# Kernel optimization log

Hardware: AMD Instinct MI355X
Metric: run time of the kernel (lower is better)

The kernel has to match this reference:

```python
import jax, jax.numpy as jnp
import numpy as np

N, F = 2048, 128
HEADS, OUT_DIM = 8, 8
ALPHA = 0.2  # tf.nn.leaky_relu default


def setup_inputs() -> dict:
    key = jax.random.key(0)
    k1, k2, k3, k4 = jax.random.split(key, 4)
    X = jax.random.normal(k1, (N, F), dtype=jnp.float32)
    A = jax.random.randint(k2, (N, N), 0, 2, dtype=jnp.int32)
    W = jax.random.normal(k3, (F, OUT_DIM * HEADS), dtype=jnp.float32) * (1.0 / np.sqrt(F))
    attn_kernel = jax.random.normal(k4, (2 * OUT_DIM, 1), dtype=jnp.float32) * 0.1
    return {"X": X, "A": A, "W": W, "attn_kernel": attn_kernel}


def reference(X, A, W, attn_kernel):
    # h: [N, heads, out_dim]
    h = (X @ W).reshape(N, HEADS, OUT_DIM)
    # tensordot(concat(h_i, h_j), a) == h_i @ a1 + h_j @ a2 (linear before leaky_relu),
    # so avoid materializing the [N,N,heads,2*out_dim] tile-concat tensor.
    a1 = attn_kernel[:OUT_DIM, 0]
    a2 = attn_kernel[OUT_DIM:, 0]
    s1 = jnp.einsum('nhd,d->nh', h, a1)  # [N, heads]
    s2 = jnp.einsum('nhd,d->nh', h, a2)  # [N, heads]
    e = jax.nn.leaky_relu(s1[:, None, :] + s2[None, :, :], ALPHA)  # [N, N, heads]
    mask = (A > 0).astype(e.dtype)[:, :, None]
    e = e * mask - 1e9 * (1.0 - mask)
    attention = jax.nn.softmax(e, axis=1)  # softmax over neighbor axis (axis=1), as in source
    # Faithful to source: einsum 'nij,njh->nih' contracts the HEAD axis
    # (attention [N,N,heads] with h [N,heads,out_dim]) -> [N, N, out_dim]
    h_prime = jnp.einsum('nij,njh->nih', attention, h)
    h_prime = h_prime.reshape(-1, OUT_DIM * HEADS)  # [N*N/heads, out_dim*heads]
    return jax.nn.leaky_relu(h_prime, ALPHA)
```

## Files before the change

### kernel.cpp

```cpp
#include <hip/hip_runtime.h>

#define NN      2048
#define FDIM    128
#define HEADS   8
#define ODIM    8
#define HID     64
#define ALPHA   0.2f

__device__ __forceinline__ float lrelu(float x) {
    return x > 0.f ? x : ALPHA * x;
}

__device__ __forceinline__ float rfl(float x) {
    return __int_as_float(__builtin_amdgcn_readfirstlane(__float_as_int(x)));
}

__global__ __launch_bounds__(64) void gat_prep(
        const float* __restrict__ X,
        const float* __restrict__ W,
        const float* __restrict__ ak,
        float* __restrict__ H,
        float* __restrict__ S1,
        float* __restrict__ S2) {
    const int n = blockIdx.x;
    const int t = threadIdx.x;

    __shared__ float Xs[FDIM];
    __shared__ float hs[HID];

    Xs[t]      = X[(size_t)n * FDIM + t];
    Xs[t + 64] = X[(size_t)n * FDIM + 64 + t];
    __syncthreads();

    float acc = 0.f;
    #pragma unroll 8
    for (int k = 0; k < FDIM; ++k)
        acc = fmaf(Xs[k], W[k * HID + t], acc);

    H[(size_t)n * HID + t] = acc;
    hs[t] = acc;
    __syncthreads();

    if (t < 16) {
        const int head = t & 7;
        const float* a = ak + ((t < 8) ? 0 : ODIM);
        float s = 0.f;
        #pragma unroll
        for (int d = 0; d < ODIM; ++d)
            s = fmaf(hs[head * ODIM + d], a[d], s);
        if (t < 8) S1[n * HEADS + head] = s;
        else       S2[n * HEADS + head] = s;
    }
}

__global__ __launch_bounds__(512, 4) void gat_fused(
        const int*   __restrict__ A,
        const float* __restrict__ H,
        const float* __restrict__ S1,
        const float* __restrict__ S2,
        float* __restrict__ out) {
    const int i    = blockIdx.x;
    const int t    = threadIdx.x;
    const int wave = t >> 6;
    const int lane = t & 63;

    __shared__ float hhS[HID];
    __shared__ float redL[8 * HEADS];
    __shared__ float LFs[HEADS];

    if (t < HID)
        hhS[t] = H[(size_t)i * HID + t];

    float s1r[HEADS];
    #pragma unroll
    for (int h = 0; h < HEADS; ++h)
        s1r[h] = rfl(S1[i * HEADS + h]);

    float p[4][HEADS];
    float ls[HEADS];
    #pragma unroll
    for (int h = 0; h < HEADS; ++h) ls[h] = 0.f;

    #pragma unroll
    for (int jj = 0; jj < 4; ++jj) {
        const int j = t + jj * 512;
        const int  msk_i = A[(size_t)i * NN + j];
        const float4 sa = *(const float4*)(S2 + j * HEADS);
        const float4 sb = *(const float4*)(S2 + j * HEADS + 4);
        const bool msk = msk_i > 0;
        const float s2v[8] = {sa.x, sa.y, sa.z, sa.w,
                              sb.x, sb.y, sb.z, sb.w};
        #pragma unroll
        for (int h = 0; h < HEADS; ++h) {
            const float x  = s1r[h] + s2v[h];
            const float pe = msk ? __expf(lrelu(x)) : 0.f;
            p[jj][h] = pe;
            ls[h]   += pe;
        }
    }

    #pragma unroll
    for (int h = 0; h < HEADS; ++h) {
        float v = ls[h];
        #pragma unroll
        for (int off = 32; off; off >>= 1)
            v += __shfl_xor(v, off);
        if (lane == 0) redL[wave * HEADS + h] = v;
    }
    __syncthreads();

    if (t < HEADS) {
        float v = 0.f;
        #pragma unroll
        for (int w = 0; w < 8; ++w)
            v += redL[w * HEADS + t];
        LFs[t] = v;
    }
    __syncthreads();

    float hh_s[HID];
    #pragma unroll
    for (int h = 0; h < HEADS; ++h) {
        const float inv = 1.0f / LFs[h];
        #pragma unroll
        for (int d = 0; d < ODIM; ++d)
            hh_s[h * ODIM + d] = rfl(hhS[h * ODIM + d] * inv);
    }

    #pragma unroll
    for (int jj = 0; jj < 4; ++jj) {
        const int j = t + jj * 512;

        float o[ODIM];
        #pragma unroll
        for (int d = 0; d < ODIM; ++d) o[d] = 0.f;
        #pragma unroll
        for (int h = 0; h < HEADS; ++h) {
            #pragma unroll
            for (int d = 0; d < ODIM; ++d)
                o[d] = fmaf(p[jj][h], hh_s[h * ODIM + d], o[d]);
        }

        const size_t base = ((size_t)i * NN + j) * ODIM;
        float4 o0, o1;
        o0.x = lrelu(o[0]); o0.y = lrelu(o[1]);
        o0.z = lrelu(o[2]); o0.w = lrelu(o[3]);
        o1.x = lrelu(o[4]); o1.y = lrelu(o[5]);
        o1.z = lrelu(o[6]); o1.w = lrelu(o[7]);
        *(float4*)(out + base)     = o0;
        *(float4*)(out + base + 4) = o1;
    }
}

extern "C" void kernel_launch(void* const* d_in, const int* in_sizes, int n_in,
                              void* d_out, int out_size, void* d_ws, size_t ws_size,
                              hipStream_t stream) {
    const float* X  = (const float*)d_in[0];
    const int*   A  = (const int*)  d_in[1];
    const float* W  = (const float*)d_in[2];
    const float* ak = (const float*)d_in[3];
    float* out = (float*)d_out;

    float* H  = (float*)d_ws;
    float* S1 = H  + (size_t)NN * HID;
    float* S2 = S1 + (size_t)NN * HEADS;

    gat_prep <<<NN,  64, 0, stream>>>(X, W, ak, H, S1, S2);
    gat_fused<<<NN, 512, 0, stream>>>(A, H, S1, S2, out);
}
```

Baseline: 185.4 us.

## Split fused attention kernel into row-sum and write kernels with finer blocks

Splits the single fused kernel into one kernel that computes the per-row softmax denominators and stores them in workspace, and another that recomputes the exponentials and writes output. The write kernel launches 8x more blocks, each thread producing one float4 of output instead of eight float4 for four columns. The aim is more parallelism and lower register pressure on the store-bound write phase. In exchange, the adjacency matrix and S2 are read twice, the exponentials are computed twice, and there is an extra kernel launch.

```diff
diff --git a/kernel.cpp b/kernel.cpp
--- a/kernel.cpp
+++ b/kernel.cpp
@@ -53,30 +53,23 @@
     }
 }
 
-__global__ __launch_bounds__(512, 4) void gat_fused(
+__global__ __launch_bounds__(512) void gat_rowsum(
         const int*   __restrict__ A,
-        const float* __restrict__ H,
         const float* __restrict__ S1,
         const float* __restrict__ S2,
-        float* __restrict__ out) {
+        float* __restrict__ LF) {
     const int i    = blockIdx.x;
     const int t    = threadIdx.x;
     const int wave = t >> 6;
     const int lane = t & 63;
 
-    __shared__ float hhS[HID];
     __shared__ float redL[8 * HEADS];
-    __shared__ float LFs[HEADS];
-
-    if (t < HID)
-        hhS[t] = H[(size_t)i * HID + t];
 
     float s1r[HEADS];
     #pragma unroll
     for (int h = 0; h < HEADS; ++h)
         s1r[h] = rfl(S1[i * HEADS + h]);
 
-    float p[4][HEADS];
     float ls[HEADS];
     #pragma unroll
     for (int h = 0; h < HEADS; ++h) ls[h] = 0.f;
@@ -84,18 +77,15 @@
     #pragma unroll
     for (int jj = 0; jj < 4; ++jj) {
         const int j = t + jj * 512;
-        const int  msk_i = A[(size_t)i * NN + j];
+        const bool msk = A[(size_t)i * NN + j] > 0;
         const float4 sa = *(const float4*)(S2 + j * HEADS);
         const float4 sb = *(const float4*)(S2 + j * HEADS + 4);
-        const bool msk = msk_i > 0;
         const float s2v[8] = {sa.x, sa.y, sa.z, sa.w,
                               sb.x, sb.y, sb.z, sb.w};
         #pragma unroll
         for (int h = 0; h < HEADS; ++h) {
-            const float x  = s1r[h] + s2v[h];
-            const float pe = msk ? __expf(lrelu(x)) : 0.f;
-            p[jj][h] = pe;
-            ls[h]   += pe;
+            const float x = s1r[h] + s2v[h];
+            ls[h] += msk ? __expf(lrelu(x)) : 0.f;
         }
     }
 
@@ -114,42 +104,63 @@
         #pragma unroll
         for (int w = 0; w < 8; ++w)
             v += redL[w * HEADS + t];
-        LFs[t] = v;
+        LF[i * HEADS + t] = v;
     }
-    __syncthreads();
+}
 
-    float hh_s[HID];
+__global__ __launch_bounds__(512) void gat_write(
+        const int*   __restrict__ A,
+        const float* __restrict__ H,
+        const float* __restrict__ S1,
+        const float* __restrict__ S2,
+        const float* __restrict__ LF,
+        float* __restrict__ out) {
+    const int bid   = blockIdx.x;
+    const int i     = bid >> 3;
+    const int chunk = bid & 7;
+    const int t     = threadIdx.x;
+    const int j     = chunk * 256 + (t >> 1);
+    const int d0    = (t & 1) * 4;
+
+    float s1r[HEADS], hh[HEADS][4];
     #pragma unroll
     for (int h = 0; h < HEADS; ++h) {
-        const float inv = 1.0f / LFs[h];
-        #pragma unroll
-        for (int d = 0; d < ODIM; ++d)
-            hh_s[h * ODIM + d] = rfl(hhS[h * ODIM + d] * inv);
+        s1r[h] = rfl(S1[i * HEADS + h]);
+        const float inv = rfl(1.0f / LF[i * HEADS + h]);
+        const float4 hv = *(const float4*)(H + (size_t)i * HID + h * ODIM + d0);
+        hh[h][0] = hv.x * inv;
+        hh[h][1] = hv.y * inv;
+        hh[h][2] = hv.z * inv;
+        hh[h][3] = hv.w * inv;
     }
 
+    const bool msk = A[(size_t)i * NN + j] > 0;
+    const float4 sa = *(const float4*)(S2 + j * HEADS);
+    const float4 sb = *(const float4*)(S2 + j * HEADS + 4);
+    const float s2v[8] = {sa.x, sa.y, sa.z, sa.w,
+                          sb.x, sb.y, sb.z, sb.w};
+
+    float p[HEADS];
     #pragma unroll
-    for (int jj = 0; jj < 4; ++jj) {
-        const int j = t + jj * 512;
+    for (int h = 0; h < HEADS; ++h) {
+        const float x = s1r[h] + s2v[h];
+        p[h] = msk ? __expf(lrelu(x)) : 0.f;
+    }
 
-        float o[ODIM];
+    float o[4];
+    #pragma unroll
+    for (int d = 0; d < 4; ++d) o[d] = 0.f;
+    #pragma unroll
+    for (int h = 0; h < HEADS; ++h) {
         #pragma unroll
-        for (int d = 0; d < ODIM; ++d) o[d] = 0.f;
-        #pragma unroll
-        for (int h = 0; h < HEADS; ++h) {
-            #pragma unroll
-            for (int d = 0; d < ODIM; ++d)
-                o[d] = fmaf(p[jj][h], hh_s[h * ODIM + d], o[d]);
-        }
+        for (int d = 0; d < 4; ++d)
+            o[d] = fmaf(p[h], hh[h][d], o[d]);
+    }
 
-        const size_t base = ((size_t)i * NN + j) * ODIM;
-        float4 o0, o1;
-        o0.x = lrelu(o[0]); o0.y = lrelu(o[1]);
-        o0.z = lrelu(o[2]); o0.w = lrelu(o[3]);
-        o1.x = lrelu(o[4]); o1.y = lrelu(o[5]);
-        o1.z = lrelu(o[6]); o1.w = lrelu(o[7]);
-        *(float4*)(out + base)     = o0;
-        *(float4*)(out + base + 4) = o1;
-    }
+    float4 ov;
+    ov.x = lrelu(o[0]); ov.y = lrelu(o[1]);
+    ov.z = lrelu(o[2]); ov.w = lrelu(o[3]);
+    *(float4*)(out + ((size_t)i * NN + j) * ODIM + d0) = ov;
 }
 
 extern "C" void kernel_launch(void* const* d_in, const int* in_sizes, int n_in,
@@ -164,7 +175,9 @@
     float* H  = (float*)d_ws;
     float* S1 = H  + (size_t)NN * HID;
     float* S2 = S1 + (size_t)NN * HEADS;
+    float* LF = S2 + (size_t)NN * HEADS;
 
-    gat_prep <<<NN,  64, 0, stream>>>(X, W, ak, H, S1, S2);
-    gat_fused<<<NN, 512, 0, stream>>>(A, H, S1, S2, out);
+    gat_prep  <<<NN,      64, 0, stream>>>(X, W, ak, H, S1, S2);
+    gat_rowsum<<<NN,     512, 0, stream>>>(A, S1, S2, LF);
+    gat_write <<<NN * 8, 512, 0, stream>>>(A, H, S1, S2, LF, out);
 }
```

Result: slower. 205.2 us (+10.7%).

## Process each attention row with a single wavefront and recompute exponentials

Applied to the files above, without the earlier changes.

The fused row kernel now uses one 64-lane wave per row instead of 512 threads. Each lane handles 32 columns, so the block-level LDS reduction and both barriers are gone and reductions are done with shuffles only. The mask is packed into a 32-bit register rather than keeping all probabilities live. The exponentials and S2 loads are recomputed in a second pass. This trades fewer barriers and less register pressure for twice the exp work, extra S2 reads, and less parallelism per block for hiding latency.

```diff
diff --git a/kernel.cpp b/kernel.cpp
--- a/kernel.cpp
+++ b/kernel.cpp
@@ -53,49 +53,38 @@
     }
 }
 
-__global__ __launch_bounds__(512, 4) void gat_fused(
+__global__ __launch_bounds__(64) void gat_row(
         const int*   __restrict__ A,
         const float* __restrict__ H,
         const float* __restrict__ S1,
         const float* __restrict__ S2,
         float* __restrict__ out) {
     const int i    = blockIdx.x;
-    const int t    = threadIdx.x;
-    const int wave = t >> 6;
-    const int lane = t & 63;
-
-    __shared__ float hhS[HID];
-    __shared__ float redL[8 * HEADS];
-    __shared__ float LFs[HEADS];
-
-    if (t < HID)
-        hhS[t] = H[(size_t)i * HID + t];
+    const int lane = threadIdx.x;
 
     float s1r[HEADS];
     #pragma unroll
     for (int h = 0; h < HEADS; ++h)
         s1r[h] = rfl(S1[i * HEADS + h]);
 
-    float p[4][HEADS];
+    unsigned int mbits = 0u;
     float ls[HEADS];
     #pragma unroll
     for (int h = 0; h < HEADS; ++h) ls[h] = 0.f;
 
-    #pragma unroll
-    for (int jj = 0; jj < 4; ++jj) {
-        const int j = t + jj * 512;
-        const int  msk_i = A[(size_t)i * NN + j];
+    #pragma unroll 8
+    for (int jj = 0; jj < 32; ++jj) {
+        const int j = lane + jj * 64;
+        const bool msk = A[(size_t)i * NN + j] > 0;
+        mbits |= (msk ? 1u : 0u) << jj;
         const float4 sa = *(const float4*)(S2 + j * HEADS);
         const float4 sb = *(const float4*)(S2 + j * HEADS + 4);
-        const bool msk = msk_i > 0;
         const float s2v[8] = {sa.x, sa.y, sa.z, sa.w,
                               sb.x, sb.y, sb.z, sb.w};
         #pragma unroll
         for (int h = 0; h < HEADS; ++h) {
-            const float x  = s1r[h] + s2v[h];
-            const float pe = msk ? __expf(lrelu(x)) : 0.f;
-            p[jj][h] = pe;
-            ls[h]   += pe;
+            const float x = s1r[h] + s2v[h];
+            ls[h] += msk ? __expf(lrelu(x)) : 0.f;
         }
     }
 
@@ -105,31 +94,40 @@
         #pragma unroll
         for (int off = 32; off; off >>= 1)
             v += __shfl_xor(v, off);
-        if (lane == 0) redL[wave * HEADS + h] = v;
+        ls[h] = v;
     }
-    __syncthreads();
 
-    if (t < HEADS) {
-        float v = 0.f;
-        #pragma unroll
-        for (int w = 0; w < 8; ++w)
-            v += redL[w * HEADS + t];
-        LFs[t] = v;
-    }
-    __syncthreads();
+    float inv_s[HEADS];
+    #pragma unroll
+    for (int h = 0; h < HEADS; ++h)
+        inv_s[h] = rfl(1.0f / ls[h]);
 
     float hh_s[HID];
     #pragma unroll
-    for (int h = 0; h < HEADS; ++h) {
-        const float inv = 1.0f / LFs[h];
-        #pragma unroll
-        for (int d = 0; d < ODIM; ++d)
-            hh_s[h * ODIM + d] = rfl(hhS[h * ODIM + d] * inv);
+    for (int k = 0; k < 16; ++k) {
+        const float4 hv = *(const float4*)(H + (size_t)i * HID + k * 4);
+        const float iv  = inv_s[k >> 1];
+        hh_s[k * 4 + 0] = rfl(hv.x * iv);
+        hh_s[k * 4 + 1] = rfl(hv.y * iv);
+        hh_s[k * 4 + 2] = rfl(hv.z * iv);
+        hh_s[k * 4 + 3] = rfl(hv.w * iv);
     }
 
-    #pragma unroll
-    for (int jj = 0; jj < 4; ++jj) {
-        const int j = t + jj * 512;
+    #pragma unroll 8
+    for (int jj = 0; jj < 32; ++jj) {
+        const int j = lane + jj * 64;
+        const bool msk = (mbits >> jj) & 1u;
+        const float4 sa = *(const float4*)(S2 + j * HEADS);
+        const float4 sb = *(const float4*)(S2 + j * HEADS + 4);
+        const float s2v[8] = {sa.x, sa.y, sa.z, sa.w,
+                              sb.x, sb.y, sb.z, sb.w};
+
+        float p[HEADS];
+        #pragma unroll
+        for (int h = 0; h < HEADS; ++h) {
+            const float x = s1r[h] + s2v[h];
+            p[h] = msk ? __expf(lrelu(x)) : 0.f;
+        }
 
         float o[ODIM];
         #pragma unroll
@@ -138,7 +136,7 @@
         for (int h = 0; h < HEADS; ++h) {
             #pragma unroll
             for (int d = 0; d < ODIM; ++d)
-                o[d] = fmaf(p[jj][h], hh_s[h * ODIM + d], o[d]);
+                o[d] = fmaf(p[h], hh_s[h * ODIM + d], o[d]);
         }
 
         const size_t base = ((size_t)i * NN + j) * ODIM;
@@ -165,6 +163,6 @@
     float* S1 = H  + (size_t)NN * HID;
     float* S2 = S1 + (size_t)NN * HEADS;
 
-    gat_prep <<<NN,  64, 0, stream>>>(X, W, ak, H, S1, S2);
-    gat_fused<<<NN, 512, 0, stream>>>(A, H, S1, S2, out);
+    gat_prep<<<NN, 64, 0, stream>>>(X, W, ak, H, S1, S2);
+    gat_row <<<NN, 64, 0, stream>>>(A, H, S1, S2, out);
 }
```

Result: slower. 190.9 us (+3.0%).
